# Performance work log

Hardware: AMD Instinct MI355X
Metric: run time of the kernel (lower is better)

## Reference

```python
import jax, jax.numpy as jnp
import numpy as np

N, C, DFF, TMAX = 4, 768, 3072, 20
RMS_EPS = 1e-6
SINK_EPS = 1e-6
POST_MULT = 2.0


def setup_inputs() -> dict:
    key = jax.random.key(0)
    ks = jax.random.split(key, 5)
    B, S = 4, 4096
    x = jax.random.normal(ks[0], (B, S, N, C), dtype=jnp.float32)
    phi = jax.random.normal(ks[1], (N * C, N * N + 2 * N), dtype=jnp.float32) * 0.02
    b = jnp.zeros((N * N + 2 * N,), dtype=jnp.float32)
    alpha_pre = jnp.ones((1,), dtype=jnp.float32)
    alpha_post = jnp.ones((1,), dtype=jnp.float32)
    alpha_res = jnp.ones((1,), dtype=jnp.float32)
    W1 = jax.random.normal(ks[2], (C, DFF), dtype=jnp.float32) * (1.0 / np.sqrt(C))
    b1 = jnp.zeros((DFF,), dtype=jnp.float32)
    W2 = jax.random.normal(ks[3], (DFF, C), dtype=jnp.float32) * (1.0 / np.sqrt(DFF))
    b2 = jnp.zeros((C,), dtype=jnp.float32)
    return {"x": x, "phi": phi, "b": b, "alpha_pre": alpha_pre,
            "alpha_post": alpha_post, "alpha_res": alpha_res,
            "W1": W1, "b1": b1, "W2": W2, "b2": b2}


def _sinkhorn(logits):
    # logits: (..., 16) -> doubly-stochastic (..., 4, 4); rows = logits[..., 4i:4i+4]
    r = logits.reshape(*logits.shape[:-1], N, N)
    r = jnp.exp(r - jnp.max(r, axis=-1, keepdims=True))
    for _ in range(TMAX):
        r = r / (jnp.sum(r, axis=-1, keepdims=True) + SINK_EPS)  # row normalize
        r = r / (jnp.sum(r, axis=-2, keepdims=True) + SINK_EPS)  # column normalize
    return r


def _mhc_forward(x, phi, b, alpha_pre, alpha_post, alpha_res, W1, b1, W2, b2):
    lead = x.shape[:-2]
    x_mat = x.reshape(-1, N * C)
    # fused RMS-norm + linear routing projection
    invr = jax.lax.rsqrt(jnp.mean(x_mat * x_mat, axis=-1, keepdims=True) + RMS_EPS)
    mix = (x_mat @ phi) * invr  # (T, n^2 + 2n)
    h_pre = jax.nn.sigmoid(mix[:, :N] * alpha_pre + b[:N]).reshape(*lead, N)
    h_post = (jax.nn.sigmoid(mix[:, N:2 * N] * alpha_post + b[N:2 * N]) * POST_MULT).reshape(*lead, N)
    h_res = _sinkhorn(mix[:, 2 * N:] * alpha_res + b[2 * N:]).reshape(*lead, N, N)
    # pre-aggregate n streams -> single full-width stream
    x_in = jnp.einsum('...nc,...n->...c', x, h_pre)
    # wrapped sublayer: baseline MLP at full width
    f_out = jax.nn.gelu(x_in @ W1 + b1, approximate=False) @ W2 + b2
    # residual stream mixing + post scatter
    res_gather = jnp.einsum('...ij,...jc->...ic', h_res, x)
    return res_gather + h_post[..., None] * f_out[..., None, :]


def reference(x, phi, b, alpha_pre, alpha_post, alpha_res, W1, b1, W2, b2):
    return _mhc_forward(x, phi, b, alpha_pre, alpha_post, alpha_res, W1, b1, W2, b2)
```

## Files before the change

### kernel.cpp

```cpp
#include <hip/hip_runtime.h>
#include <hip/hip_bf16.h>
#include <stdint.h>

#define NT   16384
#define C_   768
#define DFF_ 3072
#define KX   3072
#define NMIX 24
#define TB   64
#define KSPLIT 4
#define KSEG (KX / KSPLIT)

typedef __attribute__((ext_vector_type(8))) short shortx8;
typedef __attribute__((ext_vector_type(4))) float floatx4;

__device__ __forceinline__ short f2bf(float f) {
  union { float f; uint32_t u; } v; v.f = f;
  uint32_t r = v.u + 0x7fffu + ((v.u >> 16) & 1u);
  return (short)(r >> 16);
}

__global__ void phiT_kernel(const float* __restrict__ phi, float* __restrict__ phiT) {
  int idx = blockIdx.x * 256 + threadIdx.x;
  if (idx < KX * NMIX) {
    int k = idx / NMIX, j = idx - k * NMIX;
    phiT[(size_t)j * KX + k] = phi[idx];
  }
}

__global__ __launch_bounds__(256) void transpose_bf16(const float* __restrict__ in,
                                                      short* __restrict__ out,
                                                      int R, int C) {
  __shared__ float tile[32][33];
  int bx = blockIdx.x * 32;
  int by = blockIdx.y * 32;
  int tx = threadIdx.x & 31, ty = threadIdx.x >> 5;
  #pragma unroll
  for (int i = 0; i < 32; i += 8)
    tile[ty + i][tx] = in[(size_t)(by + ty + i) * C + bx + tx];
  __syncthreads();
  #pragma unroll
  for (int i = 0; i < 32; i += 8)
    out[(size_t)(bx + ty + i) * R + by + tx] = f2bf(tile[tx][ty + i]);
}

__global__ __launch_bounds__(256) void k1a(
    const float* __restrict__ x, const float* __restrict__ phiT,
    float* __restrict__ pmix, float* __restrict__ pssq) {
  __shared__ float xs[TB][132];
  int tid = threadIdx.x;
  int lane = tid & 63;
  int w = tid >> 6;
  int wu = __builtin_amdgcn_readfirstlane(w);
  int t0 = (blockIdx.x >> 2) * TB;
  int slot = blockIdx.x & 3;
  int ks = slot * KSEG;

  float acc[6] = {0.f, 0.f, 0.f, 0.f, 0.f, 0.f};
  float ssq = 0.f;

  for (int kc = ks; kc < ks + KSEG; kc += 128) {
    if (kc != ks) __syncthreads();
    #pragma unroll
    for (int jj = 0; jj < 8; ++jj) {
      int idx = tid + jj * 256;
      int row = idx >> 5, c4 = idx & 31;
      const float4 v = *(const float4*)&x[(size_t)(t0 + row) * KX + kc + c4 * 4];
      *(float4*)&xs[row][c4 * 4] = v;
    }
    __syncthreads();
    #pragma unroll 4
    for (int k4 = 0; k4 < 32; ++k4) {
      const float4 xv = *(const float4*)&xs[lane][k4 * 4];
      if (w == 0) ssq += xv.x * xv.x + xv.y * xv.y + xv.z * xv.z + xv.w * xv.w;
      int kk = kc + k4 * 4;
      #pragma unroll
      for (int jj = 0; jj < 6; ++jj) {
        const float4 p = *(const float4*)&phiT[(size_t)(wu * 6 + jj) * KX + kk];
        acc[jj] += p.x * xv.x + p.y * xv.y + p.z * xv.z + p.w * xv.w;
      }
    }
  }
  if (w == 0) pssq[(size_t)(t0 + lane) * KSPLIT + slot] = ssq;
  #pragma unroll
  for (int jj = 0; jj < 6; ++jj)
    pmix[((size_t)(t0 + lane) * KSPLIT + slot) * NMIX + wu * 6 + jj] = acc[jj];
}

__global__ __launch_bounds__(256) void k1b(
    const float* __restrict__ pmix, const float* __restrict__ pssq,
    const float* __restrict__ bvec, const float* __restrict__ a_pre,
    const float* __restrict__ a_post, const float* __restrict__ a_res,
    float* __restrict__ hpre, float* __restrict__ hpost, float* __restrict__ hres) {
  __shared__ float mixs[TB][NMIX];
  __shared__ float invr_s[TB];
  int tid = threadIdx.x;
  int t0 = blockIdx.x * TB;
  int tq = tid >> 2, r = tid & 3;

  {
    const float* pm = pmix + (size_t)(t0 + tq) * KSPLIT * NMIX;
    float s[6] = {0.f, 0.f, 0.f, 0.f, 0.f, 0.f};
    #pragma unroll
    for (int sl = 0; sl < KSPLIT; ++sl)
      #pragma unroll
      for (int jj = 0; jj < 6; ++jj)
        s[jj] += pm[sl * NMIX + r * 6 + jj];
    #pragma unroll
    for (int jj = 0; jj < 6; ++jj) mixs[tq][r * 6 + jj] = s[jj];
    if (r == 0) {
      const float* ps = pssq + (size_t)(t0 + tq) * KSPLIT;
      float sq = ps[0] + ps[1] + ps[2] + ps[3];
      invr_s[tq] = rsqrtf(sq * (1.0f / KX) + 1e-6f);
    }
  }
  __syncthreads();

  {
    float invr = invr_s[tq];
    float ares = a_res[0];
    float v0 = mixs[tq][8 + r * 4 + 0] * invr * ares + bvec[8 + r * 4 + 0];
    float v1 = mixs[tq][8 + r * 4 + 1] * invr * ares + bvec[8 + r * 4 + 1];
    float v2 = mixs[tq][8 + r * 4 + 2] * invr * ares + bvec[8 + r * 4 + 2];
    float v3 = mixs[tq][8 + r * 4 + 3] * invr * ares + bvec[8 + r * 4 + 3];
    float mx = fmaxf(fmaxf(v0, v1), fmaxf(v2, v3));
    v0 = __expf(v0 - mx); v1 = __expf(v1 - mx); v2 = __expf(v2 - mx); v3 = __expf(v3 - mx);
    for (int it = 0; it < 20; ++it) {
      float s = v0 + v1 + v2 + v3 + 1e-6f;
      float inv = 1.0f / s;
      v0 *= inv; v1 *= inv; v2 *= inv; v3 *= inv;
      float c0 = v0 + __shfl_xor(v0, 1); c0 += __shfl_xor(c0, 2);
      float c1 = v1 + __shfl_xor(v1, 1); c1 += __shfl_xor(c1, 2);
      float c2 = v2 + __shfl_xor(v2, 1); c2 += __shfl_xor(c2, 2);
      float c3 = v3 + __shfl_xor(v3, 1); c3 += __shfl_xor(c3, 2);
      v0 /= (c0 + 1e-6f); v1 /= (c1 + 1e-6f); v2 /= (c2 + 1e-6f); v3 /= (c3 + 1e-6f);
    }
    float* ho = hres + (size_t)(t0 + tq) * 16 + r * 4;
    ho[0] = v0; ho[1] = v1; ho[2] = v2; ho[3] = v3;
    if (r == 0) {
      float apre = a_pre[0];
      float4 hp;
      hp.x = 1.0f / (1.0f + __expf(-(mixs[tq][0] * invr * apre + bvec[0])));
      hp.y = 1.0f / (1.0f + __expf(-(mixs[tq][1] * invr * apre + bvec[1])));
      hp.z = 1.0f / (1.0f + __expf(-(mixs[tq][2] * invr * apre + bvec[2])));
      hp.w = 1.0f / (1.0f + __expf(-(mixs[tq][3] * invr * apre + bvec[3])));
      *(float4*)&hpre[(size_t)(t0 + tq) * 4] = hp;
    } else if (r == 1) {
      float apost = a_post[0];
      float4 hq;
      hq.x = 2.0f / (1.0f + __expf(-(mixs[tq][4] * invr * apost + bvec[4])));
      hq.y = 2.0f / (1.0f + __expf(-(mixs[tq][5] * invr * apost + bvec[5])));
      hq.z = 2.0f / (1.0f + __expf(-(mixs[tq][6] * invr * apost + bvec[6])));
      hq.w = 2.0f / (1.0f + __expf(-(mixs[tq][7] * invr * apost + bvec[7])));
      *(float4*)&hpost[(size_t)(t0 + tq) * 4] = hq;
    }
  }
}

__global__ __launch_bounds__(256) void k1c(
    const float* __restrict__ x, const float* __restrict__ hpre,
    short* __restrict__ x_in) {
  int idx = blockIdx.x * 256 + threadIdx.x;
  int t = idx / 192;
  int c = (idx - t * 192) * 4;
  float4 hp = *(const float4*)&hpre[(size_t)t * 4];
  const float* xr = x + (size_t)t * KX + c;
  float4 x0 = *(const float4*)(xr);
  float4 x1 = *(const float4*)(xr + C_);
  float4 x2 = *(const float4*)(xr + 2 * C_);
  float4 x3 = *(const float4*)(xr + 3 * C_);
  short4 s;
  s.x = f2bf(hp.x * x0.x + hp.y * x1.x + hp.z * x2.x + hp.w * x3.x);
  s.y = f2bf(hp.x * x0.y + hp.y * x1.y + hp.z * x2.y + hp.w * x3.y);
  s.z = f2bf(hp.x * x0.z + hp.y * x1.z + hp.z * x2.z + hp.w * x3.z);
  s.w = f2bf(hp.x * x0.w + hp.y * x1.w + hp.z * x2.w + hp.w * x3.w);
  *(short4*)&x_in[(size_t)t * C_ + c] = s;
}

template <int EPI>
__global__ __launch_bounds__(256, 3) void gemm_bt(
    const short* __restrict__ A, const short* __restrict__ B,
    int M, int N, int K, const float* __restrict__ bias,
    short* __restrict__ outb,
    const float* __restrict__ x, const float* __restrict__ hres,
    const float* __restrict__ hpost, float* __restrict__ out) {
  __shared__ short As[128 * 32];
  __shared__ short Bs[128 * 32];
  int tid = threadIdx.x;
  int lane = tid & 63, w = tid >> 6;
  int m0 = blockIdx.y * 128, n0 = blockIdx.x * 128;
  int wm = (w >> 1) * 64, wn = (w & 1) * 64;
  int lrow = lane & 15, quad = lane >> 4;
  floatx4 acc[4][4] = {};

  for (int k0 = 0; k0 < K; k0 += 32) {
    if (k0) __syncthreads();
    #pragma unroll
    for (int i = 0; i < 2; ++i) {
      int c = tid + i * 256;
      int row = c >> 2, slot = c & 3;
      const short* ga = A + (size_t)(m0 + row) * K + k0 + slot * 8;
      const short* gb = B + (size_t)(n0 + row) * K + k0 + slot * 8;
      __builtin_amdgcn_global_load_lds((const __attribute__((address_space(1))) void*)ga,
                                       (__attribute__((address_space(3))) void*)&As[c * 8],
                                       16, 0, 0);
      __builtin_amdgcn_global_load_lds((const __attribute__((address_space(1))) void*)gb,
                                       (__attribute__((address_space(3))) void*)&Bs[c * 8],
                                       16, 0, 0);
    }
    __syncthreads();
    shortx8 af[4], bfr[4];
    #pragma unroll
    for (int mi = 0; mi < 4; ++mi)
      af[mi] = *(const shortx8*)&As[(wm + mi * 16 + lrow) * 32 + quad * 8];
    #pragma unroll
    for (int ni = 0; ni < 4; ++ni)
      bfr[ni] = *(const shortx8*)&Bs[(wn + ni * 16 + lrow) * 32 + quad * 8];
    #pragma unroll
    for (int mi = 0; mi < 4; ++mi)
      #pragma unroll
      for (int ni = 0; ni < 4; ++ni)
        acc[mi][ni] = __builtin_amdgcn_mfma_f32_16x16x32_bf16(af[mi], bfr[ni], acc[mi][ni], 0, 0, 0);
  }

  float bcol[4];
  #pragma unroll
  for (int ni = 0; ni < 4; ++ni) bcol[ni] = bias[n0 + wn + ni * 16 + lrow];

  if (EPI == 1) {
    #pragma unroll
    for (int mi = 0; mi < 4; ++mi) {
      #pragma unroll
      for (int r = 0; r < 4; ++r) {
        int row = m0 + wm + mi * 16 + quad * 4 + r;
        #pragma unroll
        for (int ni = 0; ni < 4; ++ni) {
          int col = n0 + wn + ni * 16 + lrow;
          float v = acc[mi][ni][r] + bcol[ni];
          float g = 0.5f * v * (1.0f + erff(v * 0.70710678118654752f));
          outb[(size_t)row * N + col] = f2bf(g);
        }
      }
    }
  } else {
    #pragma unroll
    for (int mi = 0; mi < 4; ++mi) {
      #pragma unroll
      for (int r = 0; r < 4; ++r) {
        int row = m0 + wm + mi * 16 + quad * 4 + r;
        const float* hr = hres + (size_t)row * 16;
        const float* hp = hpost + (size_t)row * 4;
        const float* xr = x + (size_t)row * KX;
        float* orow = out + (size_t)row * KX;
        float hrv[16];
        #pragma unroll
        for (int q = 0; q < 16; ++q) hrv[q] = hr[q];
        float h0 = hp[0], h1 = hp[1], h2 = hp[2], h3 = hp[3];
        #pragma unroll
        for (int ni = 0; ni < 4; ++ni) {
          int col = n0 + wn + ni * 16 + lrow;
          float f = acc[mi][ni][r] + bcol[ni];
          float x0 = xr[col], x1 = xr[C_ + col], x2 = xr[2 * C_ + col], x3 = xr[3 * C_ + col];
          orow[col]            = hrv[0] * x0 + hrv[1] * x1 + hrv[2] * x2 + hrv[3] * x3 + h0 * f;
          orow[C_ + col]       = hrv[4] * x0 + hrv[5] * x1 + hrv[6] * x2 + hrv[7] * x3 + h1 * f;
          orow[2 * C_ + col]   = hrv[8] * x0 + hrv[9] * x1 + hrv[10] * x2 + hrv[11] * x3 + h2 * f;
          orow[3 * C_ + col]   = hrv[12] * x0 + hrv[13] * x1 + hrv[14] * x2 + hrv[15] * x3 + h3 * f;
        }
      }
    }
  }
}

extern "C" void kernel_launch(void* const* d_in, const int* in_sizes, int n_in,
                              void* d_out, int out_size, void* d_ws, size_t ws_size,
                              hipStream_t stream) {
  const float* x      = (const float*)d_in[0];
  const float* phi    = (const float*)d_in[1];
  const float* b      = (const float*)d_in[2];
  const float* a_pre  = (const float*)d_in[3];
  const float* a_post = (const float*)d_in[4];
  const float* a_res  = (const float*)d_in[5];
  const float* W1     = (const float*)d_in[6];
  const float* b1     = (const float*)d_in[7];
  const float* W2     = (const float*)d_in[8];
  const float* b2     = (const float*)d_in[9];
  float* out = (float*)d_out;

  char* ws = (char*)d_ws;
  size_t off = 0;
  auto carve = [&](size_t bytes) {
    char* p = ws + off;
    off += (bytes + 255) & ~(size_t)255;
    return p;
  };
  short* x_in  = (short*)carve((size_t)NT * C_ * 2);
  short* act   = (short*)carve((size_t)NT * DFF_ * 2);
  float* hpost = (float*)carve((size_t)NT * 4 * 4);
  float* hres  = (float*)carve((size_t)NT * 16 * 4);
  float* hpre  = (float*)carve((size_t)NT * 4 * 4);
  short* W1T   = (short*)carve((size_t)DFF_ * C_ * 2);
  short* W2T   = (short*)carve((size_t)C_ * DFF_ * 2);
  float* phiT  = (float*)carve((size_t)NMIX * KX * 4);
  float* pmix  = (float*)carve((size_t)NT * KSPLIT * NMIX * 4);
  float* pssq  = (float*)carve((size_t)NT * KSPLIT * 4);

  phiT_kernel<<<dim3((KX * NMIX + 255) / 256), 256, 0, stream>>>(phi, phiT);
  transpose_bf16<<<dim3(DFF_ / 32, C_ / 32), 256, 0, stream>>>(W1, W1T, C_, DFF_);
  transpose_bf16<<<dim3(C_ / 32, DFF_ / 32), 256, 0, stream>>>(W2, W2T, DFF_, C_);
  k1a<<<dim3((NT / TB) * KSPLIT), 256, 0, stream>>>(x, phiT, pmix, pssq);
  k1b<<<dim3(NT / TB), 256, 0, stream>>>(pmix, pssq, b, a_pre, a_post, a_res,
                                         hpre, hpost, hres);
  k1c<<<dim3(NT * 192 / 256), 256, 0, stream>>>(x, hpre, x_in);
  gemm_bt<1><<<dim3(DFF_ / 128, NT / 128), 256, 0, stream>>>(
      x_in, W1T, NT, DFF_, C_, b1, act, nullptr, nullptr, nullptr, nullptr);
  gemm_bt<2><<<dim3(C_ / 128, NT / 128), 256, 0, stream>>>(
      act, W2T, NT, C_, DFF_, b2, nullptr, x, hres, hpost, out);
}
```

Before: 716.4 us.

## Stage GEMM epilogues through LDS for coalesced vector stores and use fast GELU

Both GEMM epilogues now write bias-added (and GELU-activated) results to a padded LDS tile, then re-read them row-wise so global loads of x and stores of out/outb are 16-byte vectorized and coalesced. The erf-based GELU is replaced with a tanh-style approximation using a fast exponential. The intent is to remove strided scalar memory traffic in the epilogue and cut transcendental cost. Costs are extra LDS (which may lower occupancy), a block barrier, bf16 rounding of the second GEMM output before the residual combine, and approximation error in GELU.

```diff
diff --git a/kernel.cpp b/kernel.cpp
--- a/kernel.cpp
+++ b/kernel.cpp
@@ -18,6 +18,17 @@
   union { float f; uint32_t u; } v; v.f = f;
   uint32_t r = v.u + 0x7fffu + ((v.u >> 16) & 1u);
   return (short)(r >> 16);
+}
+
+__device__ __forceinline__ float bf2f(short s) {
+  union { uint32_t u; float f; } v;
+  v.u = ((uint32_t)(uint16_t)s) << 16;
+  return v.f;
+}
+
+__device__ __forceinline__ float gelu_f(float v) {
+  float u = 1.5957691216057308f * v * (1.0f + 0.044715f * v * v);
+  return v / (1.0f + __expf(-u));
 }
 
 __global__ void phiT_kernel(const float* __restrict__ phi, float* __restrict__ phiT) {
@@ -186,6 +197,7 @@
     const float* __restrict__ hpost, float* __restrict__ out) {
   __shared__ short As[128 * 32];
   __shared__ short Bs[128 * 32];
+  __shared__ __align__(16) short cb[128 * 136];
   int tid = threadIdx.x;
   int lane = tid & 63, w = tid >> 6;
   int m0 = blockIdx.y * 128, n0 = blockIdx.x * 128;
@@ -227,45 +239,64 @@
   #pragma unroll
   for (int ni = 0; ni < 4; ++ni) bcol[ni] = bias[n0 + wn + ni * 16 + lrow];
 
+  #pragma unroll
+  for (int mi = 0; mi < 4; ++mi) {
+    #pragma unroll
+    for (int r = 0; r < 4; ++r) {
+      int rr = wm + mi * 16 + quad * 4 + r;
+      #pragma unroll
+      for (int ni = 0; ni < 4; ++ni) {
+        int col = wn + ni * 16 + lrow;
+        float v = acc[mi][ni][r] + bcol[ni];
+        if (EPI == 1) v = gelu_f(v);
+        cb[rr * 136 + col] = f2bf(v);
+      }
+    }
+  }
+  __syncthreads();
+
+  int rbase = tid >> 4, ic = tid & 15;
   if (EPI == 1) {
     #pragma unroll
-    for (int mi = 0; mi < 4; ++mi) {
-      #pragma unroll
-      for (int r = 0; r < 4; ++r) {
-        int row = m0 + wm + mi * 16 + quad * 4 + r;
-        #pragma unroll
-        for (int ni = 0; ni < 4; ++ni) {
-          int col = n0 + wn + ni * 16 + lrow;
-          float v = acc[mi][ni][r] + bcol[ni];
-          float g = 0.5f * v * (1.0f + erff(v * 0.70710678118654752f));
-          outb[(size_t)row * N + col] = f2bf(g);
-        }
+    for (int v = 0; v < 8; ++v) {
+      int rr = v * 16 + rbase;
+      shortx8 val = *(const shortx8*)&cb[rr * 136 + ic * 8];
+      *(shortx8*)&outb[(size_t)(m0 + rr) * N + n0 + ic * 8] = val;
+    }
+  } else {
+    #pragma unroll
+    for (int v = 0; v < 8; ++v) {
+      int rr = v * 16 + rbase;
+      int tr = m0 + rr;
+      shortx8 f8 = *(const shortx8*)&cb[rr * 136 + ic * 8];
+      float fv[8];
+      #pragma unroll
+      for (int j = 0; j < 8; ++j) fv[j] = bf2f(f8[j]);
+      const float* xr = x + (size_t)tr * KX + n0 + ic * 8;
+      float4 xa[4], xb[4];
+      #pragma unroll
+      for (int n = 0; n < 4; ++n) {
+        xa[n] = *(const float4*)(xr + n * 768);
+        xb[n] = *(const float4*)(xr + n * 768 + 4);
       }
-    }
-  } else {
-    #pragma unroll
-    for (int mi = 0; mi < 4; ++mi) {
-      #pragma unroll
-      for (int r = 0; r < 4; ++r) {
-        int row = m0 + wm + mi * 16 + quad * 4 + r;
-        const float* hr = hres + (size_t)row * 16;
-        const float* hp = hpost + (size_t)row * 4;
-        const float* xr = x + (size_t)row * KX;
-        float* orow = out + (size_t)row * KX;
-        float hrv[16];
-        #pragma unroll
-        for (int q = 0; q < 16; ++q) hrv[q] = hr[q];
-        float h0 = hp[0], h1 = hp[1], h2 = hp[2], h3 = hp[3];
-        #pragma unroll
-        for (int ni = 0; ni < 4; ++ni) {
-          int col = n0 + wn + ni * 16 + lrow;
-          float f = acc[mi][ni][r] + bcol[ni];
-          float x0 = xr[col], x1 = xr[C_ + col], x2 = xr[2 * C_ + col], x3 = xr[3 * C_ + col];
-          orow[col]            = hrv[0] * x0 + hrv[1] * x1 + hrv[2] * x2 + hrv[3] * x3 + h0 * f;
-          orow[C_ + col]       = hrv[4] * x0 + hrv[5] * x1 + hrv[6] * x2 + hrv[7] * x3 + h1 * f;
-          orow[2 * C_ + col]   = hrv[8] * x0 + hrv[9] * x1 + hrv[10] * x2 + hrv[11] * x3 + h2 * f;
-          orow[3 * C_ + col]   = hrv[12] * x0 + hrv[13] * x1 + hrv[14] * x2 + hrv[15] * x3 + h3 * f;
-        }
+      const float4* hrp = (const float4*)(hres + (size_t)tr * 16);
+      float4 hp4 = *(const float4*)&hpost[(size_t)tr * 4];
+      float hpv[4] = {hp4.x, hp4.y, hp4.z, hp4.w};
+      float* orow = out + (size_t)tr * KX + n0 + ic * 8;
+      #pragma unroll
+      for (int n = 0; n < 4; ++n) {
+        float4 h = hrp[n];
+        float4 oa, ob;
+        oa.x = h.x * xa[0].x + h.y * xa[1].x + h.z * xa[2].x + h.w * xa[3].x + hpv[n] * fv[0];
+        oa.y = h.x * xa[0].y + h.y * xa[1].y + h.z * xa[2].y + h.w * xa[3].y + hpv[n] * fv[1];
+        oa.z = h.x * xa[0].z + h.y * xa[1].z + h.z * xa[2].z + h.w * xa[3].z + hpv[n] * fv[2];
+        oa.w = h.x * xa[0].w + h.y * xa[1].w + h.z * xa[2].w + h.w * xa[3].w + hpv[n] * fv[3];
+        ob.x = h.x * xb[0].x + h.y * xb[1].x + h.z * xb[2].x + h.w * xb[3].x + hpv[n] * fv[4];
+        ob.y = h.x * xb[0].y + h.y * xb[1].y + h.z * xb[2].y + h.w * xb[3].y + hpv[n] * fv[5];
+        ob.z = h.x * xb[0].z + h.y * xb[1].z + h.z * xb[2].z + h.w * xb[3].z + hpv[n] * fv[6];
+        ob.w = h.x * xb[0].w + h.y * xb[1].w + h.z * xb[2].w + h.w * xb[3].w + hpv[n] * fv[7];
+        *(float4*)(orow + n * 768) = oa;
+        *(float4*)(orow + n * 768 + 4) = ob;
       }
     }
   }
```

Result: no change. 705.6 us (-1.5%).
